# Performance work log

Hardware: AMD Instinct MI355X
Metric: run time of the kernel (lower is better)

Reference implementation:

```python
import jax, jax.numpy as jnp
import numpy as np

N_COARSE = 100_000
M_FINE = 4 * N_COARSE
GRID = 128
C_IN, C_HID, C_OUT = 32, 64, 32
K3 = 27   # 3x3x3 neighborhood
K2 = 8    # 2x2x2 transposed-conv offsets


def setup_inputs() -> dict:
    rng = np.random.default_rng(0)
    # --- sparse coarse grid: N unique voxels in GRID^3 ---
    lin = np.sort(rng.choice(GRID ** 3, size=N_COARSE, replace=False))
    cx, cy, cz = lin // (GRID * GRID), (lin // GRID) % GRID, lin % GRID
    coords = np.stack([cx, cy, cz], 1).astype(np.int64)
    # --- rulebook: neighbor index per voxel per 3^3 offset (sentinel = N) ---
    offs = np.array([(dx, dy, dz) for dx in (-1, 0, 1) for dy in (-1, 0, 1) for dz in (-1, 0, 1)])
    nbr = np.full((N_COARSE, K3), N_COARSE, np.int32)
    for k in range(K3):
        nc = coords + offs[k]
        valid = ((nc >= 0) & (nc < GRID)).all(1)
        nlin = nc[:, 0] * GRID * GRID + nc[:, 1] * GRID + nc[:, 2]
        pos = np.clip(np.searchsorted(lin, nlin), 0, N_COARSE - 1)
        found = valid & (lin[pos] == nlin)
        nbr[found, k] = pos[found].astype(np.int32)
    # --- fine grid: 4 distinct children (of 8) per coarse voxel ---
    child = np.argsort(rng.random((N_COARSE, K2)), axis=1)[:, :4].astype(np.int32)
    parent_idx = np.repeat(np.arange(N_COARSE, dtype=np.int32), 4)
    offset_idx = child.reshape(-1)

    key = jax.random.key(0)
    ks = jax.random.split(key, 16)
    nrm = lambda k, sh, fan: (jax.random.normal(k, sh, jnp.float32) / np.sqrt(fan)).astype(jnp.float32)
    return {
        "feats_in": jax.random.normal(ks[0], (N_COARSE, C_IN), jnp.float32),
        "x_up_feats": jax.random.normal(ks[1], (M_FINE, C_OUT), jnp.float32),
        "nbr_idx": jnp.asarray(nbr),
        "parent_idx": jnp.asarray(parent_idx),
        "offset_idx": jnp.asarray(offset_idx),
        "W_enc1": nrm(ks[2], (K3, C_IN, C_HID), K3 * C_IN),
        "b_enc1": jnp.zeros((C_HID,), jnp.float32),
        "W_enc2": nrm(ks[3], (K3, C_HID, C_HID), K3 * C_HID),
        "b_enc2": jnp.zeros((C_HID,), jnp.float32),
        "W_enc3": nrm(ks[4], (K3, C_HID, C_HID), K3 * C_HID),
        "b_enc3": jnp.zeros((C_HID,), jnp.float32),
        "W_t": nrm(ks[5], (K2, C_HID, C_HID), C_HID),
        "b_t": jnp.zeros((C_HID,), jnp.float32),
        "W_d1": nrm(ks[6], (C_HID, C_HID), C_HID),
        "b_d1": jnp.zeros((C_HID,), jnp.float32),
        "W_d2": nrm(ks[7], (C_HID, C_OUT), C_HID),
        "b_d2": jnp.zeros((C_OUT,), jnp.float32),
    }


def _sparse_conv3(x, nbr, W, b):
    """3x3x3 stride-1 sparse conv: gather neighbors, per-offset matmul, accumulate.
    x: [N,Cin], nbr: [N,27] (sentinel N -> zero feature), W: [27,Cin,Cout]."""
    xp = jnp.concatenate([x, jnp.zeros((1, x.shape[1]), x.dtype)], 0)  # sentinel row
    acc = jnp.broadcast_to(b, (x.shape[0], W.shape[-1]))
    for k in range(W.shape[0]):  # fixed 27-way structural loop
        acc = acc + xp[nbr[:, k]] @ W[k]
    return acc


def _t_conv2(x, parent_idx, offset_idx, W, b):
    """2x2x2 stride-2 transposed sparse conv onto a given fine grid.
    x: [N,C], parent_idx: [M] (sentinel N), offset_idx: [M] in [0,8)."""
    xp = jnp.concatenate([x, jnp.zeros((1, x.shape[1]), x.dtype)], 0)
    g = xp[parent_idx]  # [M,C]
    out = jnp.broadcast_to(b, (g.shape[0], W.shape[-1]))
    for k in range(W.shape[0]):  # fixed 8-way structural loop
        out = out + jnp.where((offset_idx == k)[:, None], g @ W[k], 0.0)
    return out


def reference(feats_in, x_up_feats, nbr_idx, parent_idx, offset_idx,
              W_enc1, b_enc1, W_enc2, b_enc2, W_enc3, b_enc3,
              W_t, b_t, W_d1, b_d1, W_d2, b_d2):
    # encoder: (conv -> dropout[eval: identity] -> relu) x 3
    x = jax.nn.relu(_sparse_conv3(feats_in, nbr_idx, W_enc1, b_enc1))
    x = jax.nn.relu(_sparse_conv3(x, nbr_idx, W_enc2, b_enc2))
    x = jax.nn.relu(_sparse_conv3(x, nbr_idx, W_enc3, b_enc3))
    # transposed upsample conv onto x_upsample's grid
    x = _t_conv2(x, parent_idx, offset_idx, W_t, b_t)
    # decoder: relu -> 1x1 conv -> relu -> 1x1 conv, then residual add
    x = jax.nn.relu(x) @ W_d1 + b_d1
    x = jax.nn.relu(x) @ W_d2 + b_d2
    return x + x_up_feats
```

## Files before the change

kernel.cpp:

```cpp
#include <hip/hip_runtime.h>
#include <hip/hip_bf16.h>

#define NC 100000
#define MF 400000
#define K3 27

typedef __bf16 bf16_t;
typedef bf16_t bf16x8 __attribute__((ext_vector_type(8)));
typedef float  f32x4  __attribute__((ext_vector_type(4)));

#define O_E1 0
#define O_E2 55296
#define O_E3 165888
#define O_T  276480
#define O_D1 309248
#define O_D2 313344
#define W_TOTAL 315392

__device__ __align__(16) bf16_t g_w[W_TOTAL];
__device__ __align__(16) bf16_t g_x0[(size_t)NC * 32];
__device__ __align__(16) bf16_t g_x1[(size_t)NC * 64];
__device__ __align__(16) bf16_t g_x2[(size_t)NC * 64];
__device__ int g_nbrT[(size_t)K3 * NC];

static __device__ __forceinline__ bf16x8 zero8() {
    bf16x8 v;
#pragma unroll
    for (int i = 0; i < 8; ++i) v[i] = (bf16_t)0.0f;
    return v;
}

__global__ __launch_bounds__(256) void prep_k(
    const float* __restrict__ W_e1, const float* __restrict__ W_e2,
    const float* __restrict__ W_e3, const float* __restrict__ W_t,
    const float* __restrict__ W_d1, const float* __restrict__ W_d2,
    const float* __restrict__ feats, const int* __restrict__ nbr)
{
    int b = blockIdx.x;
    if (b < 154) {
        int tid = b * 256 + threadIdx.x;
        int lane = tid & 63;
        int f = tid >> 6;
        const float* src; int doff, nt, nc, fb;
        if      (f < 108) { src = W_e1; doff = O_E1; nt = 4; nc = 1; fb = 0;   }
        else if (f < 324) { src = W_e2; doff = O_E2; nt = 4; nc = 2; fb = 108; }
        else if (f < 540) { src = W_e3; doff = O_E3; nt = 4; nc = 2; fb = 324; }
        else if (f < 604) { src = W_t;  doff = O_T;  nt = 4; nc = 2; fb = 540; }
        else if (f < 612) { src = W_d1; doff = O_D1; nt = 4; nc = 2; fb = 604; }
        else              { src = W_d2; doff = O_D2; nt = 2; nc = 2; fb = 612; }
        int lf = f - fb;
        int t  = lf % nt;
        int c  = (lf / nt) % nc;
        int ko = lf / (nt * nc);
        int Cin = nc * 32, Cout = nt * 16;
        int n  = t * 16 + (lane & 15);
        int kb = c * 32 + (lane >> 4) * 8;
        bf16x8 tmp;
#pragma unroll
        for (int j = 0; j < 8; ++j)
            tmp[j] = (bf16_t)src[((size_t)ko * Cin + (kb + j)) * Cout + n];
        *(bf16x8*)(g_w + doff + (size_t)lf * 512 + lane * 8) = tmp;
    } else if (b < 1717) {
        int i = (b - 154) * 256 + threadIdx.x;
        if (i < NC * 32 / 8) {
            const f32x4* p = (const f32x4*)(feats + (size_t)i * 8);
            f32x4 lo = p[0], hi = p[1];
            bf16x8 v;
#pragma unroll
            for (int j = 0; j < 4; ++j) { v[j] = (bf16_t)lo[j]; v[j + 4] = (bf16_t)hi[j]; }
            *(bf16x8*)(g_x0 + (size_t)i * 8) = v;
        }
    } else {
        int r = (b - 1717) * 256 + threadIdx.x;
        if (r < NC) {
#pragma unroll
            for (int k = 0; k < K3; ++k)
                g_nbrT[(size_t)k * NC + r] = nbr[(size_t)r * K3 + k];
        }
    }
}

#define TS 72

#define KSTEP(KO, P) do {                                                      \
    if ((KO) + 1 < K3) {                                                       \
                                \
        const bf16_t* wb_ = wsrc + (size_t)((KO) + 1) * CH * 2048 + lane * 8;  \
        _Pragma("unroll")                                                      \
        for (int c_ = 0; c_ < CH; ++c_)                                        \
            _Pragma("unroll")                                                  \
            for (int t_ = 0; t_ < 4; ++t_)                                     \
                bbuf[(P) ^ 1][c_][t_] =                                        \
                    *(const bf16x8*)(wb_ + (size_t)(c_ * 4 + t_) * 512);       \
                         \
        _Pragma("unroll")                                                      \
        for (int c_ = 0; c_ < CH; ++c_)                                        \
            _Pragma("unroll")                                                  \
            for (int mt_ = 0; mt_ < 4; ++mt_) {                                \
                int ii_ = idxbuf[(P) ^ 1][mt_];                                \
                bool va_ = (unsigned)ii_ < (unsigned)NC;                       \
                int ss_ = va_ ? ii_ : 0;                                       \
                bf16x8 a_ = *(const bf16x8*)(xb + (size_t)ss_ * CIN + c_ * 32 + q * 8); \
                if (!va_) a_ = zero8();                                        \
                abuf[(P) ^ 1][c_][mt_] = a_;                                   \
            }                                                                  \
    }                                                                          \
    if ((KO) + 2 < K3) {                                                       \
                     \
        _Pragma("unroll")                                                      \
        for (int mt_ = 0; mt_ < 4; ++mt_) {                                    \
            int r_ = base + mt_ * 16 + cl;                                     \
            idxbuf[P][mt_] = (r_ < NC) ? g_nbrT[(size_t)((KO) + 2) * NC + r_] : NC; \
        }                                                                      \
    }                                                                          \
                                       \
    _Pragma("unroll")                                                          \
    for (int c_ = 0; c_ < CH; ++c_)                                            \
        _Pragma("unroll")                                                      \
        for (int mt_ = 0; mt_ < 4; ++mt_)                                      \
            _Pragma("unroll")                                                  \
            for (int t_ = 0; t_ < 4; ++t_)                                     \
                acc[mt_][t_] = __builtin_amdgcn_mfma_f32_16x16x32_bf16(        \
                    abuf[P][c_][mt_], bbuf[P][c_][t_], acc[mt_][t_], 0, 0, 0); \
} while (0)

template <int CH>
__global__ __launch_bounds__(64, 1) void conv_k(
    int w_off,
    const float* __restrict__ bias,
    int src_sel, int dst_sel)
{
    constexpr int CIN = CH * 32;
    const bf16_t* xb = (src_sel == 0) ? g_x0 : (src_sel == 1 ? g_x1 : g_x2);
    bf16_t* y = (dst_sel == 1) ? g_x1 : g_x2;
    const bf16_t* wsrc = g_w + w_off;

    __shared__ __align__(16) bf16_t tb[2304];
    int lane = threadIdx.x & 63;
    int cl = lane & 15, q = lane >> 4;

    int per = gridDim.x >> 3;
    int blk = (blockIdx.x & 7) * per + (blockIdx.x >> 3);
    int base = blk * 64;

    int idxbuf[2][4];
    bf16x8 abuf[2][CH][4];
    bf16x8 bbuf[2][CH][4];

#pragma unroll
    for (int mt = 0; mt < 4; ++mt) {
        int r = base + mt * 16 + cl;
        idxbuf[0][mt] = (r < NC) ? g_nbrT[(size_t)0 * NC + r] : NC;
    }
    {
        const bf16_t* wb = wsrc + lane * 8;
#pragma unroll
        for (int c = 0; c < CH; ++c)
#pragma unroll
            for (int t = 0; t < 4; ++t)
                bbuf[0][c][t] = *(const bf16x8*)(wb + (size_t)(c * 4 + t) * 512);
    }
#pragma unroll
    for (int c = 0; c < CH; ++c)
#pragma unroll
        for (int mt = 0; mt < 4; ++mt) {
            int ii = idxbuf[0][mt];
            bool va = (unsigned)ii < (unsigned)NC;
            int ss = va ? ii : 0;
            bf16x8 a = *(const bf16x8*)(xb + (size_t)ss * CIN + c * 32 + q * 8);
            if (!va) a = zero8();
            abuf[0][c][mt] = a;
        }
#pragma unroll
    for (int mt = 0; mt < 4; ++mt) {
        int r = base + mt * 16 + cl;
        idxbuf[1][mt] = (r < NC) ? g_nbrT[(size_t)1 * NC + r] : NC;
    }

    f32x4 acc[4][4];
#pragma unroll
    for (int t = 0; t < 4; ++t) {
        float b = bias[t * 16 + cl];
#pragma unroll
        for (int mt = 0; mt < 4; ++mt) acc[mt][t] = (f32x4){b, b, b, b};
    }

    for (int ko = 0; ko < K3 - 1; ko += 2) {
        KSTEP(ko, 0);
        KSTEP(ko + 1, 1);
    }
    KSTEP(K3 - 1, 0);

#pragma unroll
    for (int ch = 0; ch < 2; ++ch) {
#pragma unroll
        for (int mt2 = 0; mt2 < 2; ++mt2)
#pragma unroll
            for (int t = 0; t < 4; ++t)
#pragma unroll
                for (int r = 0; r < 4; ++r) {
                    float v = acc[ch * 2 + mt2][t][r];
                    v = v > 0.0f ? v : 0.0f;
                    tb[(mt2 * 16 + q * 4 + r) * TS + t * 16 + cl] = (bf16_t)v;
                }
#pragma unroll
        for (int i = 0; i < 4; ++i) {
            int rl = i * 8 + (lane >> 3);
            int c8 = (lane & 7) * 8;
            bf16x8 v8 = *(const bf16x8*)&tb[rl * TS + c8];
            int orow = base + ch * 32 + rl;
            if (orow < NC)
                *(bf16x8*)(y + (size_t)orow * 64 + c8) = v8;
        }
    }
}

#define HS 72
__global__ __launch_bounds__(128) void tconv_dec_k(
    const int*   __restrict__ offs,
    const float* __restrict__ b_t,
    const float* __restrict__ b_d1,
    const float* __restrict__ b_d2,
    const float* __restrict__ x_up,
    float*       __restrict__ out)
{
    __shared__ __align__(16) bf16_t h_lds[2][64 * HS];
    __shared__ __align__(16) int off_lds[2][64];
    int wv = threadIdx.x >> 6, lane = threadIdx.x & 63;
    int cl = lane & 15, q = lane >> 4;
    int per = gridDim.x >> 3;
    int blk = (blockIdx.x & 7) * per + (blockIdx.x >> 3);
    int p0 = (blk * 2 + wv) * 16;
    int fbase = p0 * 4;

    {
        int fi = fbase + lane;
        off_lds[wv][lane] = (fi < MF) ? offs[fi] : 0;
    }
    int code[4];
#pragma unroll
    for (int r = 0; r < 4; ++r) {
        int4 o = *(const int4*)&off_lds[wv][(q * 4 + r) * 4];
        code[r] = (1 << (4 * o.x)) | (2 << (4 * o.y)) |
                  (3 << (4 * o.z)) | (4 << (4 * o.w));
    }

    bool pv = (p0 + cl) < NC;
    size_t xrow = (size_t)(pv ? p0 + cl : 0) * 64;
    bf16x8 ax[2];
#pragma unroll
    for (int c = 0; c < 2; ++c) {
        bf16x8 t8 = *(const bf16x8*)(g_x1 + xrow + c * 32 + q * 8);
        ax[c] = pv ? t8 : zero8();
    }

    const bf16_t* wt = g_w + O_T;
#pragma unroll
    for (int k = 0; k < 8; ++k) {
        f32x4 acc[4];
#pragma unroll
        for (int t = 0; t < 4; ++t) {
            float b = b_t[t * 16 + cl];
            acc[t] = (f32x4){b, b, b, b};
        }
#pragma unroll
        for (int c = 0; c < 2; ++c) {
            const bf16_t* wb = wt + ((size_t)(k * 2 + c) * 4) * 512 + lane * 8;
#pragma unroll
            for (int t = 0; t < 4; ++t) {
                bf16x8 b = *(const bf16x8*)(wb + t * 512);
                acc[t] = __builtin_amdgcn_mfma_f32_16x16x32_bf16(ax[c], b, acc[t], 0, 0, 0);
            }
        }
#pragma unroll
        for (int r = 0; r < 4; ++r) {
            int nib = (code[r] >> (4 * k)) & 0xF;
            if (nib) {
                int fl = (((q * 4 + r) * 4) + (nib - 1)) & 63;
#pragma unroll
                for (int t = 0; t < 4; ++t) {
                    float v = acc[t][r];
                    v = v > 0.0f ? v : 0.0f;
                    h_lds[wv][fl * HS + t * 16 + cl] = (bf16_t)v;
                }
            }
        }
    }

    bf16x8 a1[4][2];
#pragma unroll
    for (int mt = 0; mt < 4; ++mt)
#pragma unroll
        for (int c = 0; c < 2; ++c)
            a1[mt][c] = *(const bf16x8*)&h_lds[wv][(mt * 16 + cl) * HS + c * 32 + q * 8];

#pragma unroll
    for (int mt = 0; mt < 4; ++mt) {
        f32x4 acc2[4];
#pragma unroll
        for (int t = 0; t < 4; ++t) {
            float b = b_d1[t * 16 + cl];
            acc2[t] = (f32x4){b, b, b, b};
        }
#pragma unroll
        for (int c = 0; c < 2; ++c)
#pragma unroll
            for (int t = 0; t < 4; ++t) {
                bf16x8 b = *(const bf16x8*)(g_w + O_D1 + (size_t)(c * 4 + t) * 512 + lane * 8);
                acc2[t] = __builtin_amdgcn_mfma_f32_16x16x32_bf16(a1[mt][c], b, acc2[t], 0, 0, 0);
            }
#pragma unroll
        for (int t = 0; t < 4; ++t)
#pragma unroll
            for (int r = 0; r < 4; ++r) {
                float v = acc2[t][r];
                v = v > 0.0f ? v : 0.0f;
                h_lds[wv][(mt * 16 + q * 4 + r) * HS + t * 16 + cl] = (bf16_t)v;
            }
    }

    float* fW = (float*)h_lds[wv];
#pragma unroll
    for (int mt = 0; mt < 4; ++mt) {
        bf16x8 a2[2];
#pragma unroll
        for (int c = 0; c < 2; ++c)
            a2[c] = *(const bf16x8*)&h_lds[wv][(mt * 16 + cl) * HS + c * 32 + q * 8];
        f32x4 acc3[2];
#pragma unroll
        for (int t = 0; t < 2; ++t) {
            float b = b_d2[t * 16 + cl];
            acc3[t] = (f32x4){b, b, b, b};
        }
#pragma unroll
        for (int c = 0; c < 2; ++c)
#pragma unroll
            for (int t = 0; t < 2; ++t) {
                bf16x8 b = *(const bf16x8*)(g_w + O_D2 + (size_t)(c * 2 + t) * 512 + lane * 8);
                acc3[t] = __builtin_amdgcn_mfma_f32_16x16x32_bf16(a2[c], b, acc3[t], 0, 0, 0);
            }
#pragma unroll
        for (int t = 0; t < 2; ++t)
#pragma unroll
            for (int r = 0; r < 4; ++r)
                fW[(mt * 16 + q * 4 + r) * 36 + t * 16 + cl] = acc3[t][r];
    }

#pragma unroll
    for (int i = 0; i < 8; ++i) {
        int rl = i * 8 + (lane >> 3);
        int c4 = (lane & 7) * 4;
        int fg = fbase + rl;
        if (fg < MF) {
            f32x4 xv = *(const f32x4*)(x_up + (size_t)fg * 32 + c4);
            f32x4 v = *(const f32x4*)&fW[rl * 36 + c4];
            v += xv;
            *(f32x4*)(out + (size_t)fg * 32 + c4) = v;
        }
    }
}

extern "C" void kernel_launch(void* const* d_in, const int* in_sizes, int n_in,
                              void* d_out, int out_size, void* d_ws, size_t ws_size,
                              hipStream_t stream) {
    const float* feats  = (const float*)d_in[0];
    const float* x_up   = (const float*)d_in[1];
    const int*   nbr    = (const int*)d_in[2];
    const int*   offs   = (const int*)d_in[4];
    const float* W_e1 = (const float*)d_in[5];
    const float* b_e1 = (const float*)d_in[6];
    const float* W_e2 = (const float*)d_in[7];
    const float* b_e2 = (const float*)d_in[8];
    const float* W_e3 = (const float*)d_in[9];
    const float* b_e3 = (const float*)d_in[10];
    const float* W_t  = (const float*)d_in[11];
    const float* b_t  = (const float*)d_in[12];
    const float* W_d1 = (const float*)d_in[13];
    const float* b_d1 = (const float*)d_in[14];
    const float* W_d2 = (const float*)d_in[15];
    const float* b_d2 = (const float*)d_in[16];
    float* out = (float*)d_out;

    prep_k<<<2108, 256, 0, stream>>>(W_e1, W_e2, W_e3, W_t, W_d1, W_d2, feats, nbr);

    conv_k<1><<<1568, 64, 0, stream>>>(O_E1, b_e1, 0, 1);
    conv_k<2><<<1568, 64, 0, stream>>>(O_E2, b_e2, 1, 2);
    conv_k<2><<<1568, 64, 0, stream>>>(O_E3, b_e3, 2, 1);

    tconv_dec_k<<<3128, 128, 0, stream>>>(offs, b_t, b_d1, b_d2, x_up, out);
}
```

Measured before the change: 343.2 us.

## Split conv kernel offsets across two waves with LDS reduction; prefetch residual via LDS

Each conv block now runs two wavefronts that split the 27 neighbor offsets (13/14) for the same 64 rows. The partial accumulators are exchanged and summed through swizzled LDS, and each wave then writes half of the output rows. This is meant to double the waves per block and shorten the serial K loop, which only had 1568 single-wave blocks, at the cost of an LDS reduction and two barriers. The tconv/decoder kernel also issues an async global->LDS load of x_up at the start so the residual read overlaps the compute.

```diff
diff --git a/kernel.cpp b/kernel.cpp
--- a/kernel.cpp
+++ b/kernel.cpp
@@ -83,7 +83,7 @@
 #define TS 72
 
 #define KSTEP(KO, P) do {                                                      \
-    if ((KO) + 1 < K3) {                                                       \
+    if ((KO) + 1 < kend) {                                                     \
                                 \
         const bf16_t* wb_ = wsrc + (size_t)((KO) + 1) * CH * 2048 + lane * 8;  \
         _Pragma("unroll")                                                      \
@@ -105,7 +105,7 @@
                 abuf[(P) ^ 1][c_][mt_] = a_;                                   \
             }                                                                  \
     }                                                                          \
-    if ((KO) + 2 < K3) {                                                       \
+    if ((KO) + 2 < kend) {                                                     \
                      \
         _Pragma("unroll")                                                      \
         for (int mt_ = 0; mt_ < 4; ++mt_) {                                    \
@@ -125,7 +125,7 @@
 } while (0)
 
 template <int CH>
-__global__ __launch_bounds__(64, 1) void conv_k(
+__global__ __launch_bounds__(128, 2) void conv_k(
     int w_off,
     const float* __restrict__ bias,
     int src_sel, int dst_sel)
@@ -135,14 +135,19 @@
     bf16_t* y = (dst_sel == 1) ? g_x1 : g_x2;
     const bf16_t* wsrc = g_w + w_off;
 
-    __shared__ __align__(16) bf16_t tb[2304];
-    int lane = threadIdx.x & 63;
+    __shared__ __align__(16) float red[2][2048];
+
+    int tid = threadIdx.x;
+    int wv = tid >> 6, lane = tid & 63;
     int cl = lane & 15, q = lane >> 4;
 
     int per = gridDim.x >> 3;
     int blk = (blockIdx.x & 7) * per + (blockIdx.x >> 3);
     int base = blk * 64;
 
+    int kbeg = wv ? 13 : 0;
+    int kend = wv ? K3 : 13;
+
     int idxbuf[2][4];
     bf16x8 abuf[2][CH][4];
     bf16x8 bbuf[2][CH][4];
@@ -150,10 +155,10 @@
 #pragma unroll
     for (int mt = 0; mt < 4; ++mt) {
         int r = base + mt * 16 + cl;
-        idxbuf[0][mt] = (r < NC) ? g_nbrT[(size_t)0 * NC + r] : NC;
+        idxbuf[0][mt] = (r < NC) ? g_nbrT[(size_t)kbeg * NC + r] : NC;
     }
     {
-        const bf16_t* wb = wsrc + lane * 8;
+        const bf16_t* wb = wsrc + (size_t)kbeg * CH * 2048 + lane * 8;
 #pragma unroll
         for (int c = 0; c < CH; ++c)
 #pragma unroll
@@ -174,44 +179,69 @@
 #pragma unroll
     for (int mt = 0; mt < 4; ++mt) {
         int r = base + mt * 16 + cl;
-        idxbuf[1][mt] = (r < NC) ? g_nbrT[(size_t)1 * NC + r] : NC;
+        idxbuf[1][mt] = (r < NC) ? g_nbrT[(size_t)(kbeg + 1) * NC + r] : NC;
     }
 
     f32x4 acc[4][4];
 #pragma unroll
     for (int t = 0; t < 4; ++t) {
-        float b = bias[t * 16 + cl];
+        float b = wv ? 0.0f : bias[t * 16 + cl];
 #pragma unroll
         for (int mt = 0; mt < 4; ++mt) acc[mt][t] = (f32x4){b, b, b, b};
     }
 
-    for (int ko = 0; ko < K3 - 1; ko += 2) {
+    int ko = kbeg;
+    for (; ko + 1 < kend; ko += 2) {
         KSTEP(ko, 0);
         KSTEP(ko + 1, 1);
     }
-    KSTEP(K3 - 1, 0);
-
-#pragma unroll
-    for (int ch = 0; ch < 2; ++ch) {
-#pragma unroll
-        for (int mt2 = 0; mt2 < 2; ++mt2)
-#pragma unroll
-            for (int t = 0; t < 4; ++t)
-#pragma unroll
-                for (int r = 0; r < 4; ++r) {
-                    float v = acc[ch * 2 + mt2][t][r];
-                    v = v > 0.0f ? v : 0.0f;
-                    tb[(mt2 * 16 + q * 4 + r) * TS + t * 16 + cl] = (bf16_t)v;
-                }
-#pragma unroll
-        for (int i = 0; i < 4; ++i) {
-            int rl = i * 8 + (lane >> 3);
-            int c8 = (lane & 7) * 8;
-            bf16x8 v8 = *(const bf16x8*)&tb[rl * TS + c8];
-            int orow = base + ch * 32 + rl;
-            if (orow < NC)
-                *(bf16x8*)(y + (size_t)orow * 64 + c8) = v8;
-        }
+    if (ko < kend) KSTEP(ko, 0);
+
+    {
+        float* rb = red[wv];
+#pragma unroll
+        for (int m2 = 0; m2 < 2; ++m2)
+#pragma unroll
+            for (int t = 0; t < 4; ++t) {
+                int mt = (wv ? 0 : 2) + m2;
+                int k = m2 * 4 + t;
+                *(f32x4*)&rb[lane * 32 + ((k ^ (lane & 7)) << 2)] = acc[mt][t];
+            }
+    }
+    __syncthreads();
+    {
+        const float* rb = red[1 - wv];
+#pragma unroll
+        for (int m2 = 0; m2 < 2; ++m2)
+#pragma unroll
+            for (int t = 0; t < 4; ++t) {
+                int mt = wv * 2 + m2;
+                int k = m2 * 4 + t;
+                f32x4 o = *(const f32x4*)&rb[lane * 32 + ((k ^ (lane & 7)) << 2)];
+                acc[mt][t] += o;
+            }
+    }
+    __syncthreads();
+
+    bf16_t* tb = (bf16_t*)red + wv * 2304;
+#pragma unroll
+    for (int mt2 = 0; mt2 < 2; ++mt2)
+#pragma unroll
+        for (int t = 0; t < 4; ++t)
+#pragma unroll
+            for (int r = 0; r < 4; ++r) {
+                float v = acc[wv * 2 + mt2][t][r];
+                v = v > 0.0f ? v : 0.0f;
+                tb[(mt2 * 16 + q * 4 + r) * TS + t * 16 + cl] = (bf16_t)v;
+            }
+#pragma unroll
+    for (int i = 0; i < 4; ++i) {
+        int rl = i * 8 + (lane >> 3);
+        int c8 = (lane & 7) * 8;
+        bf16x8 v8 = *(const bf16x8*)&tb[rl * TS + c8];
+        int orow = base + wv * 32 + rl;
+        if (orow < NC)
+            *(bf16x8*)(y + (size_t)orow * 64 + c8) = v8;
     }
 }
 
@@ -225,7 +255,8 @@
     float*       __restrict__ out)
 {
     __shared__ __align__(16) bf16_t h_lds[2][64 * HS];
-    __shared__ __align__(16) int off_lds[2][64];
+    __shared__ __align__(16) float  xu_lds[2][2048];
+    __shared__ __align__(16) int    off_lds[2][64];
     int wv = threadIdx.x >> 6, lane = threadIdx.x & 63;
     int cl = lane & 15, q = lane >> 4;
     int per = gridDim.x >> 3;
@@ -233,6 +264,18 @@
     int p0 = (blk * 2 + wv) * 16;
     int fbase = p0 * 4;
 
+#pragma unroll
+    for (int i = 0; i < 8; ++i) {
+        int rl = i * 8 + (lane >> 3);
+        int fg = fbase + rl;
+        int srow = (fg < MF) ? fg : 0;
+        const float* gsrc = x_up + (size_t)srow * 32 + (lane & 7) * 4;
+        __builtin_amdgcn_global_load_lds(
+            (const __attribute__((address_space(1))) void*)gsrc,
+            (__attribute__((address_space(3))) void*)&xu_lds[wv][i * 256 + lane * 4],
+            16, 0, 0);
+    }
+
     {
         int fi = fbase + lane;
         off_lds[wv][lane] = (fi < MF) ? offs[fi] : 0;
@@ -346,13 +389,15 @@
                 fW[(mt * 16 + q * 4 + r) * 36 + t * 16 + cl] = acc3[t][r];
     }
 
+    asm volatile("s_waitcnt vmcnt(0)" ::: "memory");
+    __builtin_amdgcn_sched_barrier(0);
 #pragma unroll
     for (int i = 0; i < 8; ++i) {
         int rl = i * 8 + (lane >> 3);
         int c4 = (lane & 7) * 4;
         int fg = fbase + rl;
         if (fg < MF) {
-            f32x4 xv = *(const f32x4*)(x_up + (size_t)fg * 32 + c4);
+            f32x4 xv = *(const f32x4*)&xu_lds[wv][i * 256 + lane * 4];
             f32x4 v = *(const f32x4*)&fW[rl * 36 + c4];
             v += xv;
             *(f32x4*)(out + (size_t)fg * 32 + c4) = v;
@@ -383,9 +428,9 @@
 
     prep_k<<<2108, 256, 0, stream>>>(W_e1, W_e2, W_e3, W_t, W_d1, W_d2, feats, nbr);
 
-    conv_k<1><<<1568, 64, 0, stream>>>(O_E1, b_e1, 0, 1);
-    conv_k<2><<<1568, 64, 0, stream>>>(O_E2, b_e2, 1, 2);
-    conv_k<2><<<1568, 64, 0, stream>>>(O_E3, b_e3, 2, 1);
+    conv_k<1><<<1568, 128, 0, stream>>>(O_E1, b_e1, 0, 1);
+    conv_k<2><<<1568, 128, 0, stream>>>(O_E2, b_e2, 1, 2);
+    conv_k<2><<<1568, 128, 0, stream>>>(O_E3, b_e3, 2, 1);
 
     tconv_dec_k<<<3128, 128, 0, stream>>>(offs, b_t, b_d1, b_d2, x_up, out);
 }
```

New measurement: 379.9 us. 10.7% more time.
